# Optimization experiments

Hardware: AMD Instinct MI355X
Metric: run time of the kernel (lower is better)

## Reference

```python
import jax, jax.numpy as jnp
import numpy as np

# --- static index structures for the 8x8 board ---
_Dic = [[0,0],[0,1],[0,2],[0,3],[1,1],[1,2],[1,3],[2,2],[2,3],[3,3]]
_M = np.zeros((8,8), dtype=np.int32)  # param index for each board cell (4-fold reflective + transpose symmetry)
for _i, (_a, _b) in enumerate(_Dic):
    for _x, _y in [(_a,_b),(7-_a,_b),(_a,7-_b),(7-_a,7-_b)]:
        _M[_x,_y] = _i; _M[_y,_x] = _i
_xs, _ys = np.meshgrid(np.arange(8), np.arange(8), indexing='ij')
# main diagonal id i: cells with y-x=i (i<=7) or x-y=i-7 (i>7)
_main_id = np.where(_ys >= _xs, _ys - _xs, _xs - _ys + 7).reshape(-1)
# anti diagonal id i: cells with x+y=i
_anti_id = (_xs + _ys).reshape(-1)
_main_oh = jnp.asarray((np.arange(15)[None,:] == _main_id[:,None]).astype(np.float32))  # [64,15]
_anti_oh = jnp.asarray((np.arange(15)[None,:] == _anti_id[:,None]).astype(np.float32))  # [64,15]
_Mj = jnp.asarray(_M)


def setup_inputs() -> dict:
    key = jax.random.key(0)
    ks = jax.random.split(key, 11)
    B = 65536
    return {
        'state_input': jax.random.normal(ks[0], (B, 2, 8, 8), dtype=jnp.float32),
        'my_params':  jax.random.uniform(ks[1], (3, 10), dtype=jnp.float32),
        'his_params': jax.random.uniform(ks[2], (3, 10), dtype=jnp.float32),
        'w_act1': jax.random.normal(ks[3], (100, 276), dtype=jnp.float32) * 0.06,
        'b_act1': jax.random.normal(ks[4], (100,), dtype=jnp.float32) * 0.01,
        'w_act2': jax.random.normal(ks[5], (64, 100), dtype=jnp.float32) * 0.1,
        'b_act2': jax.random.normal(ks[6], (64,), dtype=jnp.float32) * 0.01,
        'w_val1': jax.random.normal(ks[7], (64, 276), dtype=jnp.float32) * 0.06,
        'b_val1': jax.random.normal(ks[8], (64,), dtype=jnp.float32) * 0.01,
        'w_val2': jax.random.normal(ks[9], (1, 64), dtype=jnp.float32) * 0.12,
        'b_val2': jax.random.normal(ks[10], (1,), dtype=jnp.float32) * 0.01,
    }


def _my_conv(state_input, my_params, his_params):
    B = state_input.shape[0]
    C = my_params.shape[0]  # 3 channels
    # D[p, j, x, y]: symmetric filter built from 10 params per plane/channel
    D = jnp.stack([my_params, his_params])[:, :, _Mj]  # [2, C, 8, 8]
    # row dots: final order is (channel j, row i, plane p)
    rows = jnp.einsum('bpiy,pjiy->bjip', state_input, D)  # [B, C, 8, 2]
    # col dots: dot(input[b,p,:,i], D[p,j,i,:])
    cols = jnp.einsum('bpxi,pjix->bjip', state_input, D)  # [B, C, 8, 2]
    # elementwise products for diagonal sums
    P = jnp.einsum('bpxy,pjxy->bjpxy', state_input, D).reshape(B, C, 2, 64)
    main = jnp.einsum('bjpn,nk->bjkp', P, _main_oh)  # [B, C, 15, 2]
    anti = jnp.einsum('bjpn,nk->bjkp', P, _anti_oh)  # [B, C, 15, 2]
    return jnp.concatenate([rows.reshape(B, -1), cols.reshape(B, -1),
                            main.reshape(B, -1), anti.reshape(B, -1)], axis=1)  # [B, 276]


def reference(state_input, my_params, his_params,
              w_act1, b_act1, w_act2, b_act2,
              w_val1, b_val1, w_val2, b_val2):
    x = jax.nn.relu(_my_conv(state_input, my_params, his_params))
    x_act = jax.nn.relu(x @ w_act1.T + b_act1)
    x_act = jax.nn.log_softmax(x_act @ w_act2.T + b_act2, axis=-1)  # [B, 64]
    x_val = jax.nn.relu(x @ w_val1.T + b_val1)
    x_val = jnp.tanh(x_val @ w_val2.T + b_val2)  # [B, 1]
    return (x_act, x_val)
```

## Files before the change

kernel.cpp:

```cpp
#include <hip/hip_runtime.h>

typedef float f32x4 __attribute__((ext_vector_type(4)));
typedef short bf16x8 __attribute__((ext_vector_type(8)));

__device__ __forceinline__ short f2bf(float f) {
    union { float f; unsigned u; } c; c.f = f;
    unsigned r = (c.u + 0x7fffu + ((c.u >> 16) & 1u)) >> 16;
    return (short)r;
}

#define XT_S 296
#define AY_S 136
#define ZL_S 68

#define DEXT_SHORTS (18*4*512)
#define W1_SHORTS   (99*512)
#define W2_SHORTS   (16*512)
#define WS2_SHORTS  (DEXT_SHORTS + W1_SHORTS + W2_SHORTS)

__device__ __forceinline__ int m8(int x, int y) {
    constexpr int M8[8][8] = {
        {0,1,2,3,3,2,1,0},{1,4,5,6,6,5,4,1},{2,5,7,8,8,7,5,2},{3,6,8,9,9,8,6,3},
        {3,6,8,9,9,8,6,3},{2,5,7,8,8,7,5,2},{1,4,5,6,6,5,4,1},{0,1,2,3,3,2,1,0}};
    return M8[x][y];
}

__global__ __launch_bounds__(256) void prep2(
    const float* __restrict__ myp,  const float* __restrict__ hisp,
    const float* __restrict__ w1a,  const float* __restrict__ w1v,
    const float* __restrict__ w2a,  short* __restrict__ ws)
{
    int i = blockIdx.x * 256 + threadIdx.x;
    if (i >= WS2_SHORTS) return;
    float v = 0.f;
    if (i < DEXT_SHORTS) {
        int e = i & 7, lane = (i >> 3) & 63, tc = i >> 9;
        int nt = tc >> 2, kc = tc & 3;
        int n = nt * 16 + (lane & 15);
        int k = kc * 32 + (lane >> 4) * 8 + e;
        int p = k >> 6, cell = k & 63, x = cell >> 3, y = cell & 7;
        const float* pr = p ? hisp : myp;
        if (n < 276) {
            bool match = false; int j = 0;
            if (n < 48)       { int p2 = n & 1, t = n >> 1; j = t >> 3; match = (p2 == p) && ((t & 7) == x); }
            else if (n < 96)  { int m = n - 48, p2 = m & 1, t = m >> 1; j = t >> 3; match = (p2 == p) && ((t & 7) == y); }
            else if (n < 186) { int m = n - 96, p2 = m & 1, t = m >> 1; j = t / 15;
                                match = (p2 == p) && ((t % 15) == ((y >= x) ? (y - x) : (x - y + 7))); }
            else              { int m = n - 186, p2 = m & 1, t = m >> 1; j = t / 15;
                                match = (p2 == p) && ((t % 15) == (x + y)); }
            if (match) v = pr[j * 10 + m8(x, y)];
        }
    } else if (i < DEXT_SHORTS + W1_SHORTS) {
        int ii = i - DEXT_SHORTS;
        int e = ii & 7, lane = (ii >> 3) & 63, tc = ii >> 9;
        int nt = tc / 9, kc = tc % 9;
        int n = nt * 16 + (lane & 15);
        int k = kc * 32 + (lane >> 4) * 8 + e;
        if (k < 276) {
            if (n < 100)                  v = w1a[n * 276 + k];
            else if (n >= 112 && n < 176) v = w1v[(n - 112) * 276 + k];
        }
    } else {
        int ii = i - DEXT_SHORTS - W1_SHORTS;
        int e = ii & 7, lane = (ii >> 3) & 63, tc = ii >> 9;
        int n = (tc >> 2) * 16 + (lane & 15);
        int k = (tc & 3) * 32 + (lane >> 4) * 8 + e;
        if (k < 100) v = w2a[n * 100 + k];
    }
    ws[i] = f2bf(v);
}

__global__ __launch_bounds__(384) void net_v3(
    const float* __restrict__ state,
    const float* __restrict__ b1a, const float* __restrict__ b2a,
    const float* __restrict__ b1v, const float* __restrict__ w2v,
    const float* __restrict__ b2v,
    const short* __restrict__ ws, float* __restrict__ out, int Btot)
{
    __shared__ __align__(16) unsigned char smem[56320];
    short* xt   = (short*)smem;
    float* zl   = (float*)smem;
    short* ay   = (short*)(smem + 37888);
    float* valp = (float*)(smem + 55296);

    const int tid  = threadIdx.x;
    const int w    = tid >> 6;
    const int l    = tid & 63;
    const int lrow = l & 15;
    const int lk   = l >> 4;
    const int bg0  = blockIdx.x * 64;

    {
        const float* sp = state + (size_t)bg0 * 128;
        #pragma unroll
        for (int it = 0; it < 6; ++it) {
            int t = tid + it * 384;
            if (t < 2048) {
                f32x4 v4 = *(const f32x4*)(sp + t * 4);
                int f = t * 4, row = f >> 7, col = f & 127;
                short* dst = ay + row * AY_S + col;
                dst[0] = f2bf(v4[0]); dst[1] = f2bf(v4[1]);
                dst[2] = f2bf(v4[2]); dst[3] = f2bf(v4[3]);
            }
        }
    }
    bf16x8 dx0[4], dx1[4], dx2[4];
    #pragma unroll
    for (int kc = 0; kc < 4; ++kc) {
        dx0[kc] = *(const bf16x8*)(ws + (((w     ) * 4 + kc) * 64 + l) * 8);
        dx1[kc] = *(const bf16x8*)(ws + (((w +  6) * 4 + kc) * 64 + l) * 8);
        dx2[kc] = *(const bf16x8*)(ws + (((w + 12) * 4 + kc) * 64 + l) * 8);
    }
    __syncthreads();

    {
        f32x4 c0[4], c1[4], c2[4];
        #pragma unroll
        for (int mt = 0; mt < 4; ++mt) {
            c0[mt] = (f32x4){0.f,0.f,0.f,0.f};
            c1[mt] = (f32x4){0.f,0.f,0.f,0.f};
            c2[mt] = (f32x4){0.f,0.f,0.f,0.f};
        }
        #pragma unroll
        for (int mt = 0; mt < 4; ++mt) {
            bf16x8 a[4];
            #pragma unroll
            for (int kc = 0; kc < 4; ++kc)
                a[kc] = *(const bf16x8*)(ay + (mt * 16 + lrow) * AY_S + kc * 32 + lk * 8);
            #pragma unroll
            for (int kc = 0; kc < 4; ++kc) {
                c0[mt] = __builtin_amdgcn_mfma_f32_16x16x32_bf16(a[kc], dx0[kc], c0[mt], 0, 0, 0);
                c1[mt] = __builtin_amdgcn_mfma_f32_16x16x32_bf16(a[kc], dx1[kc], c1[mt], 0, 0, 0);
                c2[mt] = __builtin_amdgcn_mfma_f32_16x16x32_bf16(a[kc], dx2[kc], c2[mt], 0, 0, 0);
            }
        }
        #pragma unroll
        for (int mt = 0; mt < 4; ++mt)
            #pragma unroll
            for (int r = 0; r < 4; ++r) {
                short* xr = xt + (mt * 16 + lk * 4 + r) * XT_S + lrow;
                xr[(w     ) * 16] = f2bf(fmaxf(c0[mt][r], 0.f));
                xr[(w +  6) * 16] = f2bf(fmaxf(c1[mt][r], 0.f));
                xr[(w + 12) * 16] = f2bf(fmaxf(c2[mt][r], 0.f));
            }
    }
    const bool haveB = (w < 5);
    bf16x8 bfA[9], bfB[9];
    #pragma unroll
    for (int kc = 0; kc < 9; ++kc)
        bfA[kc] = *(const bf16x8*)(ws + DEXT_SHORTS + ((w * 9 + kc) * 64 + l) * 8);
    if (haveB) {
        #pragma unroll
        for (int kc = 0; kc < 9; ++kc)
            bfB[kc] = *(const bf16x8*)(ws + DEXT_SHORTS + (((w + 6) * 9 + kc) * 64 + l) * 8);
    }
    float epbA, epbB = 0.f, epwB = 0.f;
    { const int colA = w * 16 + lrow; epbA = (colA < 100) ? b1a[colA] : 0.f; }
    if (haveB) {
        const int colB = (w + 6) * 16 + lrow;
        if (w == 0) epbB = (colB < 100) ? b1a[colB] : 0.f;
        else { epbB = b1v[colB - 112]; epwB = w2v[colB - 112]; }
    }
    __syncthreads();

    {
        f32x4 accA[4], accB[4];
        #pragma unroll
        for (int mt = 0; mt < 4; ++mt) {
            accA[mt] = (f32x4){0.f,0.f,0.f,0.f};
            accB[mt] = (f32x4){0.f,0.f,0.f,0.f};
        }
        #pragma unroll
        for (int mt = 0; mt < 4; ++mt) {
            bf16x8 a[9];
            #pragma unroll
            for (int kc = 0; kc < 9; ++kc)
                a[kc] = *(const bf16x8*)(xt + (mt * 16 + lrow) * XT_S + kc * 32 + lk * 8);
            #pragma unroll
            for (int kc = 0; kc < 9; ++kc)
                accA[mt] = __builtin_amdgcn_mfma_f32_16x16x32_bf16(a[kc], bfA[kc], accA[mt], 0, 0, 0);
            if (haveB) {
                #pragma unroll
                for (int kc = 0; kc < 9; ++kc)
                    accB[mt] = __builtin_amdgcn_mfma_f32_16x16x32_bf16(a[kc], bfB[kc], accB[mt], 0, 0, 0);
            }
        }
        #pragma unroll
        for (int mt = 0; mt < 4; ++mt)
            #pragma unroll
            for (int r = 0; r < 4; ++r) {
                float v = fmaxf(accA[mt][r] + epbA, 0.f);
                ay[(mt * 16 + lk * 4 + r) * AY_S + w * 16 + lrow] = f2bf(v);
            }
        if (haveB) {
            if (w == 0) {
                #pragma unroll
                for (int mt = 0; mt < 4; ++mt)
                    #pragma unroll
                    for (int r = 0; r < 4; ++r) {
                        const int row = mt * 16 + lk * 4 + r;
                        float v = fmaxf(accB[mt][r] + epbB, 0.f);
                        ay[row * AY_S +  96 + lrow] = f2bf(v);
                        ay[row * AY_S + 112 + lrow] = 0;
                    }
            } else {
                #pragma unroll
                for (int mt = 0; mt < 4; ++mt)
                    #pragma unroll
                    for (int r = 0; r < 4; ++r) {
                        float v = fmaxf(accB[mt][r] + epbB, 0.f) * epwB;
                        v += __shfl_xor(v, 1); v += __shfl_xor(v, 2);
                        v += __shfl_xor(v, 4); v += __shfl_xor(v, 8);
                        if (lrow == 0) valp[(w - 1) * 64 + mt * 16 + lk * 4 + r] = v;
                    }
            }
        }
    }
    bf16x8 b2f[4];
    float bias2 = 0.f;
    if (w < 4) {
        #pragma unroll
        for (int kc = 0; kc < 4; ++kc)
            b2f[kc] = *(const bf16x8*)(ws + DEXT_SHORTS + W1_SHORTS + ((w * 4 + kc) * 64 + l) * 8);
        bias2 = b2a[w * 16 + lrow];
    }
    __syncthreads();

    if (w < 4) {
        f32x4 acc2[4];
        #pragma unroll
        for (int mt = 0; mt < 4; ++mt) acc2[mt] = (f32x4){0.f,0.f,0.f,0.f};
        #pragma unroll
        for (int mt = 0; mt < 4; ++mt)
            #pragma unroll
            for (int kc = 0; kc < 4; ++kc) {
                bf16x8 a2 = *(const bf16x8*)(ay + (mt * 16 + lrow) * AY_S + kc * 32 + lk * 8);
                acc2[mt] = __builtin_amdgcn_mfma_f32_16x16x32_bf16(a2, b2f[kc], acc2[mt], 0, 0, 0);
            }
        #pragma unroll
        for (int mt = 0; mt < 4; ++mt)
            #pragma unroll
            for (int r = 0; r < 4; ++r)
                zl[(mt * 16 + lk * 4 + r) * ZL_S + w * 16 + lrow] = acc2[mt][r] + bias2;
    } else if (w == 5) {
        float v = valp[l] + valp[64 + l] + valp[128 + l] + valp[192 + l] + b2v[0];
        out[(size_t)Btot * 64 + bg0 + l] = tanhf(v);
    }
    __syncthreads();

    if (w < 4) {
        const int rl = l >> 2, q = l & 3;
        const int row = w * 16 + rl;
        const float* zr = zl + row * ZL_S;
        f32x4 v[4];
        float m = -1e30f;
        #pragma unroll
        for (int c = 0; c < 4; ++c) {
            v[c] = *(const f32x4*)(zr + c * 16 + q * 4);
            m = fmaxf(m, fmaxf(fmaxf(v[c][0], v[c][1]), fmaxf(v[c][2], v[c][3])));
        }
        m = fmaxf(m, __shfl_xor(m, 1));
        m = fmaxf(m, __shfl_xor(m, 2));
        float s = 0.f;
        #pragma unroll
        for (int c = 0; c < 4; ++c)
            #pragma unroll
            for (int e = 0; e < 4; ++e) s += __expf(v[c][e] - m);
        s += __shfl_xor(s, 1);
        s += __shfl_xor(s, 2);
        const float lsm = m + __logf(s);
        float* o = out + (size_t)(bg0 + row) * 64;
        #pragma unroll
        for (int c = 0; c < 4; ++c) {
            f32x4 ov;
            #pragma unroll
            for (int e = 0; e < 4; ++e) ov[e] = v[c][e] - lsm;
            *(f32x4*)(o + c * 16 + q * 4) = ov;
        }
    }
}

__global__ __launch_bounds__(384) void net_v1(
    const float* __restrict__ state,
    const float* __restrict__ myp,  const float* __restrict__ hisp,
    const float* __restrict__ w1a,  const float* __restrict__ b1a,
    const float* __restrict__ w2a,  const float* __restrict__ b2a,
    const float* __restrict__ w1v,  const float* __restrict__ b1v,
    const float* __restrict__ w2v,  const float* __restrict__ b2v,
    float* __restrict__ out, int Btot)
{
    __shared__ __align__(16) unsigned char smem[56320];
    short* xt   = (short*)smem;
    float* zl   = (float*)smem;
    short* ay   = (short*)(smem + 37888);
    float* valp = (float*)(smem + 55296);
    const int tid = threadIdx.x, w = tid >> 6, l = tid & 63, lrow = l & 15, lk = l >> 4;
    const int bg0 = blockIdx.x * 64;
    const bool haveB = (w < 5);

    const int cp = (w >= 3) ? 1 : 0, cj = (w >= 3) ? (w - 3) : w;
    float prm[10];
    { const float* ps = (cp == 0 ? myp : hisp) + cj * 10;
      #pragma unroll
      for (int i = 0; i < 10; i++) prm[i] = ps[i]; }
    for (int i = tid; i < 9472; i += 384) ((unsigned*)xt)[i] = 0u;
    __syncthreads();
    {
        float racc[8], cacc[8], macc[15], aacc[15];
        #pragma unroll
        for (int i = 0; i < 8; i++) { racc[i] = 0.f; cacc[i] = 0.f; }
        #pragma unroll
        for (int i = 0; i < 15; i++) { macc[i] = 0.f; aacc[i] = 0.f; }
        const float* S = state + ((size_t)(bg0 + l) * 2 + cp) * 64;
        #pragma unroll
        for (int x = 0; x < 8; x++) {
            f32x4 lo = *(const f32x4*)(S + x * 8);
            f32x4 hi = *(const f32x4*)(S + x * 8 + 4);
            #pragma unroll
            for (int y = 0; y < 8; y++) {
                float s = (y < 4) ? lo[y] : hi[y - 4];
                float t = s * prm[m8(x, y)];
                racc[x] += t; cacc[y] += t;
                macc[(y >= x) ? (y - x) : (x - y + 7)] += t;
                aacc[x + y] += t;
            }
        }
        short* xr = xt + l * XT_S;
        #pragma unroll
        for (int i = 0; i < 8; i++)  xr[(cj * 8 + i) * 2 + cp]        = f2bf(fmaxf(racc[i], 0.f));
        #pragma unroll
        for (int i = 0; i < 8; i++)  xr[48 + (cj * 8 + i) * 2 + cp]   = f2bf(fmaxf(cacc[i], 0.f));
        #pragma unroll
        for (int k = 0; k < 15; k++) xr[96 + (cj * 15 + k) * 2 + cp]  = f2bf(fmaxf(macc[k], 0.f));
        #pragma unroll
        for (int k = 0; k < 15; k++) xr[186 + (cj * 15 + k) * 2 + cp] = f2bf(fmaxf(aacc[k], 0.f));
    }
    bf16x8 bfA[9], bfB[9];
    {
        const int nA = w * 16 + lrow;
        const float* srcA = (nA < 100) ? (w1a + (size_t)nA * 276) : w1a;
        #pragma unroll
        for (int kc = 0; kc < 9; kc++) {
            bf16x8 r;
            #pragma unroll
            for (int e = 0; e < 8; e++) {
                int k = kc * 32 + lk * 8 + e;
                bool ok = (nA < 100) && (k < 276);
                r[e] = f2bf(ok ? srcA[k] : 0.f);
            }
            bfA[kc] = r;
        }
        if (haveB) {
            const int nB = (w + 6) * 16 + lrow;
            const float* srcB; bool validB;
            if (nB < 100)       { srcB = w1a + (size_t)nB * 276;         validB = true; }
            else if (nB >= 112) { srcB = w1v + (size_t)(nB - 112) * 276; validB = true; }
            else                { srcB = w1a;                            validB = false; }
            #pragma unroll
            for (int kc = 0; kc < 9; kc++) {
                bf16x8 r;
                #pragma unroll
                for (int e = 0; e < 8; e++) {
                    int k = kc * 32 + lk * 8 + e;
                    bool ok = validB && (k < 276);
                    r[e] = f2bf(ok ? srcB[k] : 0.f);
                }
                bfB[kc] = r;
            }
        }
    }
    float epbA, epbB = 0.f, epwB = 0.f;
    { const int colA = w * 16 + lrow; epbA = (colA < 100) ? b1a[colA] : 0.f; }
    if (haveB) {
        const int colB = (w + 6) * 16 + lrow;
        if (w == 0) epbB = (colB < 100) ? b1a[colB] : 0.f;
        else { epbB = b1v[colB - 112]; epwB = w2v[colB - 112]; }
    }
    __syncthreads();
    {
        f32x4 accA[4], accB[4];
        #pragma unroll
        for (int mt = 0; mt < 4; ++mt) {
            accA[mt] = (f32x4){0.f,0.f,0.f,0.f};
            accB[mt] = (f32x4){0.f,0.f,0.f,0.f};
        }
        #pragma unroll
        for (int mt = 0; mt < 4; ++mt) {
            bf16x8 a[9];
            #pragma unroll
            for (int kc = 0; kc < 9; ++kc)
                a[kc] = *(const bf16x8*)(xt + (mt * 16 + lrow) * XT_S + kc * 32 + lk * 8);
            #pragma unroll
            for (int kc = 0; kc < 9; ++kc)
                accA[mt] = __builtin_amdgcn_mfma_f32_16x16x32_bf16(a[kc], bfA[kc], accA[mt], 0, 0, 0);
            if (haveB) {
                #pragma unroll
                for (int kc = 0; kc < 9; ++kc)
                    accB[mt] = __builtin_amdgcn_mfma_f32_16x16x32_bf16(a[kc], bfB[kc], accB[mt], 0, 0, 0);
            }
        }
        #pragma unroll
        for (int mt = 0; mt < 4; ++mt)
            #pragma unroll
            for (int r = 0; r < 4; ++r) {
                float v = fmaxf(accA[mt][r] + epbA, 0.f);
                ay[(mt * 16 + lk * 4 + r) * AY_S + w * 16 + lrow] = f2bf(v);
            }
        if (haveB) {
            if (w == 0) {
                #pragma unroll
                for (int mt = 0; mt < 4; ++mt)
                    #pragma unroll
                    for (int r = 0; r < 4; ++r) {
                        const int row = mt * 16 + lk * 4 + r;
                        float v = fmaxf(accB[mt][r] + epbB, 0.f);
                        ay[row * AY_S +  96 + lrow] = f2bf(v);
                        ay[row * AY_S + 112 + lrow] = 0;
                    }
            } else {
                #pragma unroll
                for (int mt = 0; mt < 4; ++mt)
                    #pragma unroll
                    for (int r = 0; r < 4; ++r) {
                        float v = fmaxf(accB[mt][r] + epbB, 0.f) * epwB;
                        v += __shfl_xor(v, 1); v += __shfl_xor(v, 2);
                        v += __shfl_xor(v, 4); v += __shfl_xor(v, 8);
                        if (lrow == 0) valp[(w - 1) * 64 + mt * 16 + lk * 4 + r] = v;
                    }
            }
        }
    }
    bf16x8 b2f[4];
    float bias2 = 0.f;
    if (w < 4) {
        const float* src2 = w2a + (size_t)(w * 16 + lrow) * 100;
        #pragma unroll
        for (int kc = 0; kc < 4; kc++) {
            bf16x8 r;
            #pragma unroll
            for (int e = 0; e < 8; e++) { int k = kc * 32 + lk * 8 + e; r[e] = f2bf((k < 100) ? src2[k] : 0.f); }
            b2f[kc] = r;
        }
        bias2 = b2a[w * 16 + lrow];
    }
    __syncthreads();
    if (w < 4) {
        f32x4 acc2[4];
        #pragma unroll
        for (int mt = 0; mt < 4; ++mt) acc2[mt] = (f32x4){0.f,0.f,0.f,0.f};
        #pragma unroll
        for (int mt = 0; mt < 4; ++mt)
            #pragma unroll
            for (int kc = 0; kc < 4; ++kc) {
                bf16x8 a2 = *(const bf16x8*)(ay + (mt * 16 + lrow) * AY_S + kc * 32 + lk * 8);
                acc2[mt] = __builtin_amdgcn_mfma_f32_16x16x32_bf16(a2, b2f[kc], acc2[mt], 0, 0, 0);
            }
        #pragma unroll
        for (int mt = 0; mt < 4; ++mt)
            #pragma unroll
            for (int r = 0; r < 4; ++r)
                zl[(mt * 16 + lk * 4 + r) * ZL_S + w * 16 + lrow] = acc2[mt][r] + bias2;
    } else if (w == 5) {
        float v = valp[l] + valp[64 + l] + valp[128 + l] + valp[192 + l] + b2v[0];
        out[(size_t)Btot * 64 + bg0 + l] = tanhf(v);
    }
    __syncthreads();
    if (w < 4) {
        const int rl = l >> 2, q = l & 3;
        const int row = w * 16 + rl;
        const float* zr = zl + row * ZL_S;
        f32x4 v[4]; float m = -1e30f;
        #pragma unroll
        for (int c = 0; c < 4; ++c) {
            v[c] = *(const f32x4*)(zr + c * 16 + q * 4);
            m = fmaxf(m, fmaxf(fmaxf(v[c][0], v[c][1]), fmaxf(v[c][2], v[c][3])));
        }
        m = fmaxf(m, __shfl_xor(m, 1));
        m = fmaxf(m, __shfl_xor(m, 2));
        float s = 0.f;
        #pragma unroll
        for (int c = 0; c < 4; ++c)
            #pragma unroll
            for (int e = 0; e < 4; ++e) s += __expf(v[c][e] - m);
        s += __shfl_xor(s, 1);
        s += __shfl_xor(s, 2);
        const float lsm = m + __logf(s);
        float* o = out + (size_t)(bg0 + row) * 64;
        #pragma unroll
        for (int c = 0; c < 4; ++c) {
            f32x4 ov;
            #pragma unroll
            for (int e = 0; e < 4; ++e) ov[e] = v[c][e] - lsm;
            *(f32x4*)(o + c * 16 + q * 4) = ov;
        }
    }
}

extern "C" void kernel_launch(void* const* d_in, const int* in_sizes, int n_in,
                              void* d_out, int out_size, void* d_ws, size_t ws_size,
                              hipStream_t stream) {
    const float* state = (const float*)d_in[0];
    const float* myp   = (const float*)d_in[1];
    const float* hisp  = (const float*)d_in[2];
    const float* w1a   = (const float*)d_in[3];
    const float* b1a   = (const float*)d_in[4];
    const float* w2a   = (const float*)d_in[5];
    const float* b2a   = (const float*)d_in[6];
    const float* w1v   = (const float*)d_in[7];
    const float* b1v   = (const float*)d_in[8];
    const float* w2v   = (const float*)d_in[9];
    const float* b2v   = (const float*)d_in[10];
    float* out = (float*)d_out;
    const int Btot = in_sizes[0] / 128;
    const int blocks = Btot / 64;
    if (ws_size >= (size_t)WS2_SHORTS * sizeof(short)) {
        short* ws = (short*)d_ws;
        prep2<<<dim3((WS2_SHORTS + 255) / 256), dim3(256), 0, stream>>>(myp, hisp, w1a, w1v, w2a, ws);
        net_v3<<<dim3(blocks), dim3(384), 0, stream>>>(
            state, b1a, b2a, b1v, w2v, b2v, ws, out, Btot);
    } else {
        net_v1<<<dim3(blocks), dim3(384), 0, stream>>>(
            state, myp, hisp, w1a, b1a, w2a, b2a, w1v, b1v, w2v, b2v, out, Btot);
    }
}
```

Measured before the change: 46.19 us.

## Halve per-block batch tile to 32 rows for higher occupancy

Each block now handles 32 boards instead of 64. That halves shared memory to about 28KB and halves the accumulator register arrays, and a launch-bounds hint asks for 6 blocks per CU. The softmax epilogue is reorganized so 8 lanes cover one row, and the log-sum-exp is broadcast by shuffle so output rows are written as contiguous 64-float stores. The goal is more resident waves to hide latency. In exchange, each block reloads the full bf16 weight set from global or L2 for half as many rows, which doubles total weight traffic.

```diff
diff --git a/kernel.cpp b/kernel.cpp
--- a/kernel.cpp
+++ b/kernel.cpp
@@ -70,32 +70,32 @@
     ws[i] = f2bf(v);
 }
 
-__global__ __launch_bounds__(384) void net_v3(
+__global__ __launch_bounds__(384, 6) void net_v4(
     const float* __restrict__ state,
     const float* __restrict__ b1a, const float* __restrict__ b2a,
     const float* __restrict__ b1v, const float* __restrict__ w2v,
     const float* __restrict__ b2v,
     const short* __restrict__ ws, float* __restrict__ out, int Btot)
 {
-    __shared__ __align__(16) unsigned char smem[56320];
+    __shared__ __align__(16) unsigned char smem[28160];
     short* xt   = (short*)smem;
     float* zl   = (float*)smem;
-    short* ay   = (short*)(smem + 37888);
-    float* valp = (float*)(smem + 55296);
+    short* ay   = (short*)(smem + 18944);
+    float* valp = (float*)(smem + 27648);
 
     const int tid  = threadIdx.x;
     const int w    = tid >> 6;
     const int l    = tid & 63;
     const int lrow = l & 15;
     const int lk   = l >> 4;
-    const int bg0  = blockIdx.x * 64;
+    const int bg0  = blockIdx.x * 32;
 
     {
         const float* sp = state + (size_t)bg0 * 128;
         #pragma unroll
-        for (int it = 0; it < 6; ++it) {
+        for (int it = 0; it < 3; ++it) {
             int t = tid + it * 384;
-            if (t < 2048) {
+            if (t < 1024) {
                 f32x4 v4 = *(const f32x4*)(sp + t * 4);
                 int f = t * 4, row = f >> 7, col = f & 127;
                 short* dst = ay + row * AY_S + col;
@@ -114,15 +114,15 @@
     __syncthreads();
 
     {
-        f32x4 c0[4], c1[4], c2[4];
-        #pragma unroll
-        for (int mt = 0; mt < 4; ++mt) {
+        f32x4 c0[2], c1[2], c2[2];
+        #pragma unroll
+        for (int mt = 0; mt < 2; ++mt) {
             c0[mt] = (f32x4){0.f,0.f,0.f,0.f};
             c1[mt] = (f32x4){0.f,0.f,0.f,0.f};
             c2[mt] = (f32x4){0.f,0.f,0.f,0.f};
         }
         #pragma unroll
-        for (int mt = 0; mt < 4; ++mt) {
+        for (int mt = 0; mt < 2; ++mt) {
             bf16x8 a[4];
             #pragma unroll
             for (int kc = 0; kc < 4; ++kc)
@@ -135,7 +135,7 @@
             }
         }
         #pragma unroll
-        for (int mt = 0; mt < 4; ++mt)
+        for (int mt = 0; mt < 2; ++mt)
             #pragma unroll
             for (int r = 0; r < 4; ++r) {
                 short* xr = xt + (mt * 16 + lk * 4 + r) * XT_S + lrow;
@@ -164,14 +164,14 @@
     __syncthreads();
 
     {
-        f32x4 accA[4], accB[4];
-        #pragma unroll
-        for (int mt = 0; mt < 4; ++mt) {
+        f32x4 accA[2], accB[2];
+        #pragma unroll
+        for (int mt = 0; mt < 2; ++mt) {
             accA[mt] = (f32x4){0.f,0.f,0.f,0.f};
             accB[mt] = (f32x4){0.f,0.f,0.f,0.f};
         }
         #pragma unroll
-        for (int mt = 0; mt < 4; ++mt) {
+        for (int mt = 0; mt < 2; ++mt) {
             bf16x8 a[9];
             #pragma unroll
             for (int kc = 0; kc < 9; ++kc)
@@ -186,7 +186,7 @@
             }
         }
         #pragma unroll
-        for (int mt = 0; mt < 4; ++mt)
+        for (int mt = 0; mt < 2; ++mt)
             #pragma unroll
             for (int r = 0; r < 4; ++r) {
                 float v = fmaxf(accA[mt][r] + epbA, 0.f);
@@ -195,7 +195,7 @@
         if (haveB) {
             if (w == 0) {
                 #pragma unroll
-                for (int mt = 0; mt < 4; ++mt)
+                for (int mt = 0; mt < 2; ++mt)
                     #pragma unroll
                     for (int r = 0; r < 4; ++r) {
                         const int row = mt * 16 + lk * 4 + r;
@@ -205,13 +205,13 @@
                     }
             } else {
                 #pragma unroll
-                for (int mt = 0; mt < 4; ++mt)
+                for (int mt = 0; mt < 2; ++mt)
                     #pragma unroll
                     for (int r = 0; r < 4; ++r) {
                         float v = fmaxf(accB[mt][r] + epbB, 0.f) * epwB;
                         v += __shfl_xor(v, 1); v += __shfl_xor(v, 2);
                         v += __shfl_xor(v, 4); v += __shfl_xor(v, 8);
-                        if (lrow == 0) valp[(w - 1) * 64 + mt * 16 + lk * 4 + r] = v;
+                        if (lrow == 0) valp[(w - 1) * 32 + mt * 16 + lk * 4 + r] = v;
                     }
             }
         }
@@ -227,55 +227,57 @@
     __syncthreads();
 
     if (w < 4) {
-        f32x4 acc2[4];
-        #pragma unroll
-        for (int mt = 0; mt < 4; ++mt) acc2[mt] = (f32x4){0.f,0.f,0.f,0.f};
-        #pragma unroll
-        for (int mt = 0; mt < 4; ++mt)
+        f32x4 acc2[2];
+        #pragma unroll
+        for (int mt = 0; mt < 2; ++mt) acc2[mt] = (f32x4){0.f,0.f,0.f,0.f};
+        #pragma unroll
+        for (int mt = 0; mt < 2; ++mt)
             #pragma unroll
             for (int kc = 0; kc < 4; ++kc) {
                 bf16x8 a2 = *(const bf16x8*)(ay + (mt * 16 + lrow) * AY_S + kc * 32 + lk * 8);
                 acc2[mt] = __builtin_amdgcn_mfma_f32_16x16x32_bf16(a2, b2f[kc], acc2[mt], 0, 0, 0);
             }
         #pragma unroll
-        for (int mt = 0; mt < 4; ++mt)
+        for (int mt = 0; mt < 2; ++mt)
             #pragma unroll
             for (int r = 0; r < 4; ++r)
                 zl[(mt * 16 + lk * 4 + r) * ZL_S + w * 16 + lrow] = acc2[mt][r] + bias2;
-    } else if (w == 5) {
-        float v = valp[l] + valp[64 + l] + valp[128 + l] + valp[192 + l] + b2v[0];
+    } else if (w == 5 && l < 32) {
+        float v = valp[l] + valp[32 + l] + valp[64 + l] + valp[96 + l] + b2v[0];
         out[(size_t)Btot * 64 + bg0 + l] = tanhf(v);
     }
     __syncthreads();
 
     if (w < 4) {
-        const int rl = l >> 2, q = l & 3;
-        const int row = w * 16 + rl;
-        const float* zr = zl + row * ZL_S;
-        f32x4 v[4];
-        float m = -1e30f;
-        #pragma unroll
-        for (int c = 0; c < 4; ++c) {
-            v[c] = *(const f32x4*)(zr + c * 16 + q * 4);
-            m = fmaxf(m, fmaxf(fmaxf(v[c][0], v[c][1]), fmaxf(v[c][2], v[c][3])));
-        }
+        const int rl = l >> 3, q = l & 7;
+        const int row = w * 8 + rl;
+        const float* zr = zl + row * ZL_S + q * 8;
+        f32x4 v0 = *(const f32x4*)(zr);
+        f32x4 v1 = *(const f32x4*)(zr + 4);
+        float m = fmaxf(fmaxf(fmaxf(v0[0], v0[1]), fmaxf(v0[2], v0[3])),
+                        fmaxf(fmaxf(v1[0], v1[1]), fmaxf(v1[2], v1[3])));
         m = fmaxf(m, __shfl_xor(m, 1));
         m = fmaxf(m, __shfl_xor(m, 2));
+        m = fmaxf(m, __shfl_xor(m, 4));
         float s = 0.f;
         #pragma unroll
-        for (int c = 0; c < 4; ++c)
-            #pragma unroll
-            for (int e = 0; e < 4; ++e) s += __expf(v[c][e] - m);
+        for (int e = 0; e < 4; ++e) s += __expf(v0[e] - m);
+        #pragma unroll
+        for (int e = 0; e < 4; ++e) s += __expf(v1[e] - m);
         s += __shfl_xor(s, 1);
         s += __shfl_xor(s, 2);
+        s += __shfl_xor(s, 4);
         const float lsm = m + __logf(s);
-        float* o = out + (size_t)(bg0 + row) * 64;
-        #pragma unroll
-        for (int c = 0; c < 4; ++c) {
+        #pragma unroll
+        for (int i = 0; i < 2; ++i) {
+            const int rloc  = i * 4 + (l >> 4);
+            const int row_s = w * 8 + rloc;
+            const float lz  = __shfl(lsm, rloc * 8);
+            f32x4 zv = *(const f32x4*)(zl + row_s * ZL_S + (l & 15) * 4);
             f32x4 ov;
             #pragma unroll
-            for (int e = 0; e < 4; ++e) ov[e] = v[c][e] - lsm;
-            *(f32x4*)(o + c * 16 + q * 4) = ov;
+            for (int e = 0; e < 4; ++e) ov[e] = zv[e] - lz;
+            *(f32x4*)(out + (size_t)(bg0 + row_s) * 64 + (l & 15) * 4) = ov;
         }
     }
 }
@@ -512,14 +514,13 @@
     const float* b2v   = (const float*)d_in[10];
     float* out = (float*)d_out;
     const int Btot = in_sizes[0] / 128;
-    const int blocks = Btot / 64;
     if (ws_size >= (size_t)WS2_SHORTS * sizeof(short)) {
         short* ws = (short*)d_ws;
         prep2<<<dim3((WS2_SHORTS + 255) / 256), dim3(256), 0, stream>>>(myp, hisp, w1a, w1v, w2a, ws);
-        net_v3<<<dim3(blocks), dim3(384), 0, stream>>>(
+        net_v4<<<dim3(Btot / 32), dim3(384), 0, stream>>>(
             state, b1a, b2a, b1v, w2v, b2v, ws, out, Btot);
     } else {
-        net_v1<<<dim3(blocks), dim3(384), 0, stream>>>(
+        net_v1<<<dim3(Btot / 64), dim3(384), 0, stream>>>(
             state, myp, hisp, w1a, b1a, w2a, b2a, w1v, b1v, w2v, b2v, out, Btot);
     }
 }
```

Result: slower. 107.4 us (+132.6%).

## Process two 64-row tiles per block and pack conv outputs via transposed MFMA

Applied to the files above, without the earlier changes.

Each block now loops over MPB=2 consecutive 64-sample tiles, so the grid is halved and bias and scalar loads are hoisted out of the per-tile work. The first conv MFMA swaps its A and B operands to produce a transposed accumulator layout. That layout lets each lane write its four results as two packed 32-bit bf16x2 LDS stores instead of twelve scalar short stores. The trade-off is fewer blocks in flight, which may reduce latency hiding, and serialised tiles within a block.

```diff
diff --git a/kernel.cpp b/kernel.cpp
--- a/kernel.cpp
+++ b/kernel.cpp
@@ -8,10 +8,14 @@
     unsigned r = (c.u + 0x7fffu + ((c.u >> 16) & 1u)) >> 16;
     return (short)r;
 }
+__device__ __forceinline__ unsigned pk2(float a, float b) {
+    return (unsigned)(unsigned short)f2bf(a) | ((unsigned)(unsigned short)f2bf(b) << 16);
+}
 
 #define XT_S 296
 #define AY_S 136
 #define ZL_S 68
+#define MPB 2
 
 #define DEXT_SHORTS (18*4*512)
 #define W1_SHORTS   (99*512)
@@ -70,7 +74,7 @@
     ws[i] = f2bf(v);
 }
 
-__global__ __launch_bounds__(384) void net_v3(
+__global__ __launch_bounds__(384) void net_v10(
     const float* __restrict__ state,
     const float* __restrict__ b1a, const float* __restrict__ b2a,
     const float* __restrict__ b1v, const float* __restrict__ w2v,
@@ -88,194 +92,203 @@
     const int l    = tid & 63;
     const int lrow = l & 15;
     const int lk   = l >> 4;
-    const int bg0  = blockIdx.x * 64;
-
-    {
-        const float* sp = state + (size_t)bg0 * 128;
-        #pragma unroll
-        for (int it = 0; it < 6; ++it) {
-            int t = tid + it * 384;
-            if (t < 2048) {
-                f32x4 v4 = *(const f32x4*)(sp + t * 4);
-                int f = t * 4, row = f >> 7, col = f & 127;
-                short* dst = ay + row * AY_S + col;
-                dst[0] = f2bf(v4[0]); dst[1] = f2bf(v4[1]);
-                dst[2] = f2bf(v4[2]); dst[3] = f2bf(v4[3]);
-            }
-        }
-    }
-    bf16x8 dx0[4], dx1[4], dx2[4];
-    #pragma unroll
-    for (int kc = 0; kc < 4; ++kc) {
-        dx0[kc] = *(const bf16x8*)(ws + (((w     ) * 4 + kc) * 64 + l) * 8);
-        dx1[kc] = *(const bf16x8*)(ws + (((w +  6) * 4 + kc) * 64 + l) * 8);
-        dx2[kc] = *(const bf16x8*)(ws + (((w + 12) * 4 + kc) * 64 + l) * 8);
-    }
-    __syncthreads();
-
-    {
-        f32x4 c0[4], c1[4], c2[4];
-        #pragma unroll
-        for (int mt = 0; mt < 4; ++mt) {
-            c0[mt] = (f32x4){0.f,0.f,0.f,0.f};
-            c1[mt] = (f32x4){0.f,0.f,0.f,0.f};
-            c2[mt] = (f32x4){0.f,0.f,0.f,0.f};
-        }
-        #pragma unroll
-        for (int mt = 0; mt < 4; ++mt) {
-            bf16x8 a[4];
-            #pragma unroll
-            for (int kc = 0; kc < 4; ++kc)
-                a[kc] = *(const bf16x8*)(ay + (mt * 16 + lrow) * AY_S + kc * 32 + lk * 8);
-            #pragma unroll
-            for (int kc = 0; kc < 4; ++kc) {
-                c0[mt] = __builtin_amdgcn_mfma_f32_16x16x32_bf16(a[kc], dx0[kc], c0[mt], 0, 0, 0);
-                c1[mt] = __builtin_amdgcn_mfma_f32_16x16x32_bf16(a[kc], dx1[kc], c1[mt], 0, 0, 0);
-                c2[mt] = __builtin_amdgcn_mfma_f32_16x16x32_bf16(a[kc], dx2[kc], c2[mt], 0, 0, 0);
-            }
-        }
-        #pragma unroll
-        for (int mt = 0; mt < 4; ++mt)
-            #pragma unroll
-            for (int r = 0; r < 4; ++r) {
-                short* xr = xt + (mt * 16 + lk * 4 + r) * XT_S + lrow;
-                xr[(w     ) * 16] = f2bf(fmaxf(c0[mt][r], 0.f));
-                xr[(w +  6) * 16] = f2bf(fmaxf(c1[mt][r], 0.f));
-                xr[(w + 12) * 16] = f2bf(fmaxf(c2[mt][r], 0.f));
-            }
-    }
     const bool haveB = (w < 5);
-    bf16x8 bfA[9], bfB[9];
-    #pragma unroll
-    for (int kc = 0; kc < 9; ++kc)
-        bfA[kc] = *(const bf16x8*)(ws + DEXT_SHORTS + ((w * 9 + kc) * 64 + l) * 8);
-    if (haveB) {
-        #pragma unroll
-        for (int kc = 0; kc < 9; ++kc)
-            bfB[kc] = *(const bf16x8*)(ws + DEXT_SHORTS + (((w + 6) * 9 + kc) * 64 + l) * 8);
-    }
-    float epbA, epbB = 0.f, epwB = 0.f;
+
+    float epbA, epbB = 0.f, epwB = 0.f, bias2 = 0.f;
     { const int colA = w * 16 + lrow; epbA = (colA < 100) ? b1a[colA] : 0.f; }
     if (haveB) {
         const int colB = (w + 6) * 16 + lrow;
         if (w == 0) epbB = (colB < 100) ? b1a[colB] : 0.f;
         else { epbB = b1v[colB - 112]; epwB = w2v[colB - 112]; }
     }
-    __syncthreads();
-
-    {
-        f32x4 accA[4], accB[4];
-        #pragma unroll
-        for (int mt = 0; mt < 4; ++mt) {
-            accA[mt] = (f32x4){0.f,0.f,0.f,0.f};
-            accB[mt] = (f32x4){0.f,0.f,0.f,0.f};
-        }
-        #pragma unroll
-        for (int mt = 0; mt < 4; ++mt) {
-            bf16x8 a[9];
+    if (w < 4) bias2 = b2a[w * 16 + lrow];
+    const float b2v0 = b2v[0];
+
+    for (int g = 0; g < MPB; ++g) {
+        const int bg0 = (blockIdx.x * MPB + g) * 64;
+        if (bg0 >= Btot) break;
+
+        {
+            const float* sp = state + (size_t)bg0 * 128;
+            #pragma unroll
+            for (int it = 0; it < 6; ++it) {
+                int t = tid + it * 384;
+                if (t < 2048) {
+                    f32x4 v4 = *(const f32x4*)(sp + t * 4);
+                    int f = t * 4, row = f >> 7, col = f & 127;
+                    short* dst = ay + row * AY_S + col;
+                    dst[0] = f2bf(v4[0]); dst[1] = f2bf(v4[1]);
+                    dst[2] = f2bf(v4[2]); dst[3] = f2bf(v4[3]);
+                }
+            }
+        }
+        bf16x8 dx0[4], dx1[4], dx2[4];
+        #pragma unroll
+        for (int kc = 0; kc < 4; ++kc) {
+            dx0[kc] = *(const bf16x8*)(ws + (((w     ) * 4 + kc) * 64 + l) * 8);
+            dx1[kc] = *(const bf16x8*)(ws + (((w +  6) * 4 + kc) * 64 + l) * 8);
+            dx2[kc] = *(const bf16x8*)(ws + (((w + 12) * 4 + kc) * 64 + l) * 8);
+        }
+        __syncthreads();
+
+        {
+            f32x4 c0[4], c1[4], c2[4];
+            #pragma unroll
+            for (int mt = 0; mt < 4; ++mt) {
+                c0[mt] = (f32x4){0.f,0.f,0.f,0.f};
+                c1[mt] = (f32x4){0.f,0.f,0.f,0.f};
+                c2[mt] = (f32x4){0.f,0.f,0.f,0.f};
+            }
+            #pragma unroll
+            for (int mt = 0; mt < 4; ++mt) {
+                bf16x8 a[4];
+                #pragma unroll
+                for (int kc = 0; kc < 4; ++kc)
+                    a[kc] = *(const bf16x8*)(ay + (mt * 16 + lrow) * AY_S + kc * 32 + lk * 8);
+                #pragma unroll
+                for (int kc = 0; kc < 4; ++kc) {
+                    c0[mt] = __builtin_amdgcn_mfma_f32_16x16x32_bf16(dx0[kc], a[kc], c0[mt], 0, 0, 0);
+                    c1[mt] = __builtin_amdgcn_mfma_f32_16x16x32_bf16(dx1[kc], a[kc], c1[mt], 0, 0, 0);
+                    c2[mt] = __builtin_amdgcn_mfma_f32_16x16x32_bf16(dx2[kc], a[kc], c2[mt], 0, 0, 0);
+                }
+            }
+            #pragma unroll
+            for (int mt = 0; mt < 4; ++mt) {
+                short* xr = xt + (mt * 16 + lrow) * XT_S + lk * 4;
+                unsigned* d0 = (unsigned*)(xr + (w     ) * 16);
+                d0[0] = pk2(fmaxf(c0[mt][0], 0.f), fmaxf(c0[mt][1], 0.f));
+                d0[1] = pk2(fmaxf(c0[mt][2], 0.f), fmaxf(c0[mt][3], 0.f));
+                unsigned* d1 = (unsigned*)(xr + (w +  6) * 16);
+                d1[0] = pk2(fmaxf(c1[mt][0], 0.f), fmaxf(c1[mt][1], 0.f));
+                d1[1] = pk2(fmaxf(c1[mt][2], 0.f), fmaxf(c1[mt][3], 0.f));
+                unsigned* d2 = (unsigned*)(xr + (w + 12) * 16);
+                d2[0] = pk2(fmaxf(c2[mt][0], 0.f), fmaxf(c2[mt][1], 0.f));
+                d2[1] = pk2(fmaxf(c2[mt][2], 0.f), fmaxf(c2[mt][3], 0.f));
+            }
+        }
+        bf16x8 bfA[9], bfB[9];
+        #pragma unroll
+        for (int kc = 0; kc < 9; ++kc)
+            bfA[kc] = *(const bf16x8*)(ws + DEXT_SHORTS + ((w * 9 + kc) * 64 + l) * 8);
+        if (haveB) {
             #pragma unroll
             for (int kc = 0; kc < 9; ++kc)
-                a[kc] = *(const bf16x8*)(xt + (mt * 16 + lrow) * XT_S + kc * 32 + lk * 8);
-            #pragma unroll
-            for (int kc = 0; kc < 9; ++kc)
-                accA[mt] = __builtin_amdgcn_mfma_f32_16x16x32_bf16(a[kc], bfA[kc], accA[mt], 0, 0, 0);
+                bfB[kc] = *(const bf16x8*)(ws + DEXT_SHORTS + (((w + 6) * 9 + kc) * 64 + l) * 8);
+        }
+        __syncthreads();
+
+        {
+            f32x4 accA[4], accB[4];
+            #pragma unroll
+            for (int mt = 0; mt < 4; ++mt) {
+                accA[mt] = (f32x4){0.f,0.f,0.f,0.f};
+                accB[mt] = (f32x4){0.f,0.f,0.f,0.f};
+            }
+            #pragma unroll
+            for (int mt = 0; mt < 4; ++mt) {
+                bf16x8 a[9];
+                #pragma unroll
+                for (int kc = 0; kc < 9; ++kc)
+                    a[kc] = *(const bf16x8*)(xt + (mt * 16 + lrow) * XT_S + kc * 32 + lk * 8);
+                #pragma unroll
+                for (int kc = 0; kc < 9; ++kc)
+                    accA[mt] = __builtin_amdgcn_mfma_f32_16x16x32_bf16(a[kc], bfA[kc], accA[mt], 0, 0, 0);
+                if (haveB) {
+                    #pragma unroll
+                    for (int kc = 0; kc < 9; ++kc)
+                        accB[mt] = __builtin_amdgcn_mfma_f32_16x16x32_bf16(a[kc], bfB[kc], accB[mt], 0, 0, 0);
+                }
+            }
+            #pragma unroll
+            for (int mt = 0; mt < 4; ++mt)
+                #pragma unroll
+                for (int r = 0; r < 4; ++r) {
+                    float v = fmaxf(accA[mt][r] + epbA, 0.f);
+                    ay[(mt * 16 + lk * 4 + r) * AY_S + w * 16 + lrow] = f2bf(v);
+                }
             if (haveB) {
-                #pragma unroll
-                for (int kc = 0; kc < 9; ++kc)
-                    accB[mt] = __builtin_amdgcn_mfma_f32_16x16x32_bf16(a[kc], bfB[kc], accB[mt], 0, 0, 0);
-            }
-        }
-        #pragma unroll
-        for (int mt = 0; mt < 4; ++mt)
-            #pragma unroll
-            for (int r = 0; r < 4; ++r) {
-                float v = fmaxf(accA[mt][r] + epbA, 0.f);
-                ay[(mt * 16 + lk * 4 + r) * AY_S + w * 16 + lrow] = f2bf(v);
-            }
-        if (haveB) {
-            if (w == 0) {
-                #pragma unroll
-                for (int mt = 0; mt < 4; ++mt)
+                if (w == 0) {
                     #pragma unroll
-                    for (int r = 0; r < 4; ++r) {
-                        const int row = mt * 16 + lk * 4 + r;
-                        float v = fmaxf(accB[mt][r] + epbB, 0.f);
-                        ay[row * AY_S +  96 + lrow] = f2bf(v);
-                        ay[row * AY_S + 112 + lrow] = 0;
-                    }
-            } else {
-                #pragma unroll
-                for (int mt = 0; mt < 4; ++mt)
+                    for (int mt = 0; mt < 4; ++mt)
+                        #pragma unroll
+                        for (int r = 0; r < 4; ++r) {
+                            const int row = mt * 16 + lk * 4 + r;
+                            float v = fmaxf(accB[mt][r] + epbB, 0.f);
+                            ay[row * AY_S +  96 + lrow] = f2bf(v);
+                            ay[row * AY_S + 112 + lrow] = 0;
+                        }
+                } else {
                     #pragma unroll
-                    for (int r = 0; r < 4; ++r) {
-                        float v = fmaxf(accB[mt][r] + epbB, 0.f) * epwB;
-                        v += __shfl_xor(v, 1); v += __shfl_xor(v, 2);
-                        v += __shfl_xor(v, 4); v += __shfl_xor(v, 8);
-                        if (lrow == 0) valp[(w - 1) * 64 + mt * 16 + lk * 4 + r] = v;
-                    }
-            }
-        }
-    }
-    bf16x8 b2f[4];
-    float bias2 = 0.f;
-    if (w < 4) {
-        #pragma unroll
-        for (int kc = 0; kc < 4; ++kc)
-            b2f[kc] = *(const bf16x8*)(ws + DEXT_SHORTS + W1_SHORTS + ((w * 4 + kc) * 64 + l) * 8);
-        bias2 = b2a[w * 16 + lrow];
-    }
-    __syncthreads();
-
-    if (w < 4) {
-        f32x4 acc2[4];
-        #pragma unroll
-        for (int mt = 0; mt < 4; ++mt) acc2[mt] = (f32x4){0.f,0.f,0.f,0.f};
-        #pragma unroll
-        for (int mt = 0; mt < 4; ++mt)
-            #pragma unroll
-            for (int kc = 0; kc < 4; ++kc) {
-                bf16x8 a2 = *(const bf16x8*)(ay + (mt * 16 + lrow) * AY_S + kc * 32 + lk * 8);
-                acc2[mt] = __builtin_amdgcn_mfma_f32_16x16x32_bf16(a2, b2f[kc], acc2[mt], 0, 0, 0);
-            }
-        #pragma unroll
-        for (int mt = 0; mt < 4; ++mt)
-            #pragma unroll
-            for (int r = 0; r < 4; ++r)
-                zl[(mt * 16 + lk * 4 + r) * ZL_S + w * 16 + lrow] = acc2[mt][r] + bias2;
-    } else if (w == 5) {
-        float v = valp[l] + valp[64 + l] + valp[128 + l] + valp[192 + l] + b2v[0];
-        out[(size_t)Btot * 64 + bg0 + l] = tanhf(v);
-    }
-    __syncthreads();
-
-    if (w < 4) {
-        const int rl = l >> 2, q = l & 3;
-        const int row = w * 16 + rl;
-        const float* zr = zl + row * ZL_S;
-        f32x4 v[4];
-        float m = -1e30f;
-        #pragma unroll
-        for (int c = 0; c < 4; ++c) {
-            v[c] = *(const f32x4*)(zr + c * 16 + q * 4);
-            m = fmaxf(m, fmaxf(fmaxf(v[c][0], v[c][1]), fmaxf(v[c][2], v[c][3])));
-        }
-        m = fmaxf(m, __shfl_xor(m, 1));
-        m = fmaxf(m, __shfl_xor(m, 2));
-        float s = 0.f;
-        #pragma unroll
-        for (int c = 0; c < 4; ++c)
-            #pragma unroll
-            for (int e = 0; e < 4; ++e) s += __expf(v[c][e] - m);
-        s += __shfl_xor(s, 1);
-        s += __shfl_xor(s, 2);
-        const float lsm = m + __logf(s);
-        float* o = out + (size_t)(bg0 + row) * 64;
-        #pragma unroll
-        for (int c = 0; c < 4; ++c) {
-            f32x4 ov;
-            #pragma unroll
-            for (int e = 0; e < 4; ++e) ov[e] = v[c][e] - lsm;
-            *(f32x4*)(o + c * 16 + q * 4) = ov;
+                    for (int mt = 0; mt < 4; ++mt)
+                        #pragma unroll
+                        for (int r = 0; r < 4; ++r) {
+                            float v = fmaxf(accB[mt][r] + epbB, 0.f) * epwB;
+                            v += __shfl_xor(v, 1); v += __shfl_xor(v, 2);
+                            v += __shfl_xor(v, 4); v += __shfl_xor(v, 8);
+                            if (lrow == 0) valp[(w - 1) * 64 + mt * 16 + lk * 4 + r] = v;
+                        }
+                }
+            }
+        }
+        bf16x8 b2f[4];
+        if (w < 4) {
+            #pragma unroll
+            for (int kc = 0; kc < 4; ++kc)
+                b2f[kc] = *(const bf16x8*)(ws + DEXT_SHORTS + W1_SHORTS + ((w * 4 + kc) * 64 + l) * 8);
+        }
+        __syncthreads();
+
+        if (w < 4) {
+            f32x4 acc2[4];
+            #pragma unroll
+            for (int mt = 0; mt < 4; ++mt) acc2[mt] = (f32x4){0.f,0.f,0.f,0.f};
+            #pragma unroll
+            for (int mt = 0; mt < 4; ++mt)
+                #pragma unroll
+                for (int kc = 0; kc < 4; ++kc) {
+                    bf16x8 a2 = *(const bf16x8*)(ay + (mt * 16 + lrow) * AY_S + kc * 32 + lk * 8);
+                    acc2[mt] = __builtin_amdgcn_mfma_f32_16x16x32_bf16(a2, b2f[kc], acc2[mt], 0, 0, 0);
+                }
+            #pragma unroll
+            for (int mt = 0; mt < 4; ++mt)
+                #pragma unroll
+                for (int r = 0; r < 4; ++r)
+                    zl[(mt * 16 + lk * 4 + r) * ZL_S + w * 16 + lrow] = acc2[mt][r] + bias2;
+        } else if (w == 5) {
+            float v = valp[l] + valp[64 + l] + valp[128 + l] + valp[192 + l] + b2v0;
+            out[(size_t)Btot * 64 + bg0 + l] = tanhf(v);
+        }
+        __syncthreads();
+
+        if (w < 4) {
+            const int rl = l >> 2, q = l & 3;
+            const int row = w * 16 + rl;
+            const float* zr = zl + row * ZL_S;
+            f32x4 v[4];
+            float m = -1e30f;
+            #pragma unroll
+            for (int c = 0; c < 4; ++c) {
+                v[c] = *(const f32x4*)(zr + c * 16 + q * 4);
+                m = fmaxf(m, fmaxf(fmaxf(v[c][0], v[c][1]), fmaxf(v[c][2], v[c][3])));
+            }
+            m = fmaxf(m, __shfl_xor(m, 1));
+            m = fmaxf(m, __shfl_xor(m, 2));
+            float s = 0.f;
+            #pragma unroll
+            for (int c = 0; c < 4; ++c)
+                #pragma unroll
+                for (int e = 0; e < 4; ++e) s += __expf(v[c][e] - m);
+            s += __shfl_xor(s, 1);
+            s += __shfl_xor(s, 2);
+            const float lsm = m + __logf(s);
+            float* o = out + (size_t)(bg0 + row) * 64;
+            #pragma unroll
+            for (int c = 0; c < 4; ++c) {
+                f32x4 ov;
+                #pragma unroll
+                for (int e = 0; e < 4; ++e) ov[e] = v[c][e] - lsm;
+                *(f32x4*)(o + c * 16 + q * 4) = ov;
+            }
         }
     }
 }
@@ -297,7 +310,6 @@
     const int tid = threadIdx.x, w = tid >> 6, l = tid & 63, lrow = l & 15, lk = l >> 4;
     const int bg0 = blockIdx.x * 64;
     const bool haveB = (w < 5);
-
     const int cp = (w >= 3) ? 1 : 0, cj = (w >= 3) ? (w - 3) : w;
     float prm[10];
     { const float* ps = (cp == 0 ? myp : hisp) + cj * 10;
@@ -512,14 +524,13 @@
     const float* b2v   = (const float*)d_in[10];
     float* out = (float*)d_out;
     const int Btot = in_sizes[0] / 128;
-    const int blocks = Btot / 64;
     if (ws_size >= (size_t)WS2_SHORTS * sizeof(short)) {
         short* ws = (short*)d_ws;
         prep2<<<dim3((WS2_SHORTS + 255) / 256), dim3(256), 0, stream>>>(myp, hisp, w1a, w1v, w2a, ws);
-        net_v3<<<dim3(blocks), dim3(384), 0, stream>>>(
+        net_v10<<<dim3((Btot + 64 * MPB - 1) / (64 * MPB)), dim3(384), 0, stream>>>(
             state, b1a, b2a, b1v, w2v, b2v, ws, out, Btot);
     } else {
-        net_v1<<<dim3(blocks), dim3(384), 0, stream>>>(
+        net_v1<<<dim3(Btot / 64), dim3(384), 0, stream>>>(
             state, myp, hisp, w1a, b1a, w2a, b2a, w1v, b1v, w2v, b2v, out, Btot);
     }
 }
```

Result: slower. 48.43 us (+4.9%).
